# Optimization experiments

Hardware: AMD Instinct MI355X
Metric: run time of the kernel (lower is better)

Reference implementation:

```python
import jax, jax.numpy as jnp
import numpy as np

B, T = 8, 4096
EMBED_DIM = 128
ENGRAM_EMBED_DIM = 64
VOCAB_SIZES = [4096, 4096]
MAX_NGRAM = 3
NUM_HEADS = 2
N_STREAMS = 4
KERNEL = 4
TOTAL_NGRAMS = len(VOCAB_SIZES) * NUM_HEADS          # 4
INPUT_DIM = TOTAL_NGRAMS * ENGRAM_EMBED_DIM          # 256
TOTAL_SLOTS = sum(VOCAB_SIZES) * NUM_HEADS           # 16384


def setup_inputs() -> dict:
    key = jax.random.key(0)
    ks = jax.random.split(key, 10)
    x = jax.random.normal(ks[0], (B, T, N_STREAMS, EMBED_DIM), dtype=jnp.float32)
    input_ids = jax.random.randint(ks[1], (B, T), 0, 50257, dtype=jnp.int32)
    multipliers = jax.random.randint(ks[2], (MAX_NGRAM - 1, NUM_HEADS, MAX_NGRAM), 1, 10000, dtype=jnp.int32)
    embedding = jax.random.normal(ks[3], (TOTAL_SLOTS, ENGRAM_EMBED_DIM), dtype=jnp.float32) * 0.02
    val_W = jax.random.normal(ks[4], (EMBED_DIM, INPUT_DIM), dtype=jnp.float32) * 0.05
    val_b = jnp.zeros((EMBED_DIM,), jnp.float32)
    key_W = jax.random.normal(ks[5], (N_STREAMS, EMBED_DIM, INPUT_DIM), dtype=jnp.float32) * 0.05
    key_b = jnp.zeros((N_STREAMS, EMBED_DIM), jnp.float32)
    normq_w = jnp.ones((N_STREAMS, EMBED_DIM), jnp.float32)
    normk_w = jnp.ones((N_STREAMS, EMBED_DIM), jnp.float32)
    conv_w = jax.random.normal(ks[6], (N_STREAMS * EMBED_DIM, 1, KERNEL), dtype=jnp.float32) * 0.1
    convnorm_w = jnp.ones((N_STREAMS, EMBED_DIM), jnp.float32)
    return {"x": x, "input_ids": input_ids, "multipliers": multipliers,
            "embedding": embedding, "val_W": val_W, "val_b": val_b,
            "key_W": key_W, "key_b": key_b, "normq_w": normq_w,
            "normk_w": normk_w, "conv_w": conv_w, "convnorm_w": convnorm_w}


def rmsnorm(v, w):
    # torch nn.RMSNorm default eps = finfo(dtype).eps
    eps = jnp.finfo(v.dtype).eps
    return v * jax.lax.rsqrt(jnp.mean(v * v, axis=-1, keepdims=True) + eps) * w


def hash_ids_fn(input_ids, multipliers):
    padded = jnp.pad(input_ids, ((0, 0), (MAX_NGRAM - 1, 0)))            # [B, T+2]
    windows = jnp.stack([padded[:, i:i + T] for i in range(MAX_NGRAM)], axis=-1)  # [B,T,3]
    hashes = []
    for n_idx in range(MAX_NGRAM - 1):
        ngram_len = n_idx + 2
        grams = windows[:, :, MAX_NGRAM - ngram_len:]                    # [B,T,L]
        mults = multipliers[n_idx, :, :ngram_len]                        # [H,L]
        mixed = grams[:, :, None, :] * mults[None, None, :, :]           # [B,T,H,L]
        h = mixed[..., 0]
        for k in range(1, ngram_len):
            h = jnp.bitwise_xor(h, mixed[..., k])
        hashes.append(h % VOCAB_SIZES[n_idx])                            # [B,T,H]
    return jnp.concatenate(hashes, axis=2)                               # [B,T,4]


def engram_forward(x, input_ids, multipliers, embedding, val_W, val_b,
                   key_W, key_b, normq_w, normk_w, conv_w, convnorm_w):
    hids = hash_ids_fn(input_ids, multipliers)
    offsets = jnp.cumsum(jnp.array([0] + [v for v in VOCAB_SIZES for _ in range(NUM_HEADS)], jnp.int32))[:-1]
    ids = hids + offsets                                                 # [B,T,4]
    emb = embedding[ids].reshape(B, T, INPUT_DIM)                        # [B,T,256]
    v_base = emb @ val_W.T + val_b                                       # [B,T,128]
    k = rmsnorm(jnp.einsum('bte,gde->btgd', emb, key_W) + key_b, normk_w)  # [B,T,G,D]
    q = rmsnorm(x, normq_w)                                              # [B,T,G,D]
    score = jnp.sum(q * k, axis=-1, keepdims=True) / (EMBED_DIM ** 0.5)
    gates = jax.nn.sigmoid(score)                                        # [B,T,G,1]
    v_gated = v_base[:, :, None, :] * gates                              # [B,T,G,D]
    # ShortConv: per-chunk RMSNorm -> causal depthwise conv -> SiLU
    xn = rmsnorm(v_gated, convnorm_w).reshape(B, T, N_STREAMS * EMBED_DIM)
    x_bct = jnp.transpose(xn, (0, 2, 1))                                 # [B,C,T]
    x_bct = jnp.pad(x_bct, ((0, 0), (0, 0), (KERNEL - 1, 0)))            # causal left pad
    y_bct = jax.lax.conv_general_dilated(
        x_bct, conv_w, window_strides=(1,), padding='VALID',
        dimension_numbers=('NCH', 'OIH', 'NCH'),
        feature_group_count=N_STREAMS * EMBED_DIM)                       # [B,C,T]
    y = jax.nn.silu(y_bct)
    y = jnp.transpose(y, (0, 2, 1)).reshape(B, T, N_STREAMS, EMBED_DIM)
    return v_gated + y


def reference(x, input_ids, multipliers, embedding, val_W, val_b,
              key_W, key_b, normq_w, normk_w, conv_w, convnorm_w):
    return engram_forward(x, input_ids, multipliers, embedding, val_W, val_b,
                          key_W, key_b, normq_w, normk_w, conv_w, convnorm_w)
```

## Files before the change

### kernel.cpp

```cpp
#include <hip/hip_runtime.h>
#include <math.h>

#define EPS 1.1920928955078125e-07f

typedef __attribute__((ext_vector_type(8)))  short short8;
typedef __attribute__((ext_vector_type(4)))  short short4v;
typedef __attribute__((ext_vector_type(16))) float floatx16;

__device__ __forceinline__ float4 ld4(const float* __restrict__ p) { return *(const float4* __restrict__)p; }
__device__ __forceinline__ void   st4(float* __restrict__ p, float4 v) { *(float4* __restrict__)p = v; }

__device__ __forceinline__ unsigned short f2bf(float f) {
    union { float f; unsigned u; } v; v.f = f;
    unsigned r = v.u + 0x7fffu + ((v.u >> 16) & 1u);
    return (unsigned short)(r >> 16);
}

__global__ __launch_bounds__(256) void build_wb(const float* __restrict__ val_W,
                                                const float* __restrict__ key_W,
                                                unsigned short* __restrict__ WbF)
{
    int idx  = blockIdx.x * 256 + threadIdx.x;
    int lane = idx & 63;
    int ks   = (idx >> 6) & 15;
    int nt   = idx >> 10;
    int n = (nt << 5) + (lane & 31);
    int k = (ks << 4) + ((lane >> 5) << 3);
    const float* src = (n < 512) ? key_W + (size_t)n * 256 + k
                                 : val_W + (size_t)(n - 512) * 256 + k;
    float4 v0 = ld4(src), v1 = ld4(src + 4);
    unsigned short o[8] = { f2bf(v0.x), f2bf(v0.y), f2bf(v0.z), f2bf(v0.w),
                            f2bf(v1.x), f2bf(v1.y), f2bf(v1.z), f2bf(v1.w) };
    unsigned short* dst = WbF + (size_t)idx * 8;
    *(short4v*)dst       = *(short4v*)&o[0];
    *(short4v*)(dst + 4) = *(short4v*)&o[4];
}

__global__ __launch_bounds__(256) void engram_gemm(
    const float* __restrict__ x,
    const int*   __restrict__ input_ids,
    const int*   __restrict__ mult,
    const float* __restrict__ embedding,
    const float* __restrict__ val_b,
    const float* __restrict__ key_b,
    const float* __restrict__ normq_w,
    const float* __restrict__ normk_w,
    const unsigned short* __restrict__ WbF,
    float* __restrict__ v_base,
    float* __restrict__ Gbuf,
    float* __restrict__ S2buf)
{
    __shared__ int   sids[64][4];
    __shared__ short AD[64 * 260];

    const int tid  = threadIdx.x;
    const int bid  = blockIdx.x;
    const int c    = bid % 5;
    const int tok0 = (bid / 5) << 6;

    if (tid < 64) {
        int token = tok0 + tid;
        int b = token >> 12, t = token & 4095;
        const int* row = input_ids + (b << 12);
        unsigned g2 = (unsigned)row[t];
        unsigned g1 = (t >= 1) ? (unsigned)row[t - 1] : 0u;
        unsigned g0 = (t >= 2) ? (unsigned)row[t - 2] : 0u;
        sids[tid][0] = (int)(((g1 * (unsigned)mult[0]) ^ (g2 * (unsigned)mult[1])) & 4095u);
        sids[tid][1] = (int)((((g1 * (unsigned)mult[3]) ^ (g2 * (unsigned)mult[4])) & 4095u) + 4096u);
        sids[tid][2] = (int)((((g0 * (unsigned)mult[6]) ^ (g1 * (unsigned)mult[7]) ^ (g2 * (unsigned)mult[8])) & 4095u) + 8192u);
        sids[tid][3] = (int)((((g0 * (unsigned)mult[9]) ^ (g1 * (unsigned)mult[10]) ^ (g2 * (unsigned)mult[11])) & 4095u) + 12288u);
    }
    __syncthreads();

    #pragma unroll
    for (int it = 0; it < 4; ++it) {
        int f = it * 256 + tid;
        int token = f >> 4, seg = f & 15;
        const float* src = embedding + ((size_t)sids[token][seg >> 2] << 6) + ((seg & 3) << 4);
        short* dst = AD + token * 260 + (seg << 4);
        #pragma unroll
        for (int i = 0; i < 4; ++i) {
            float4 v = ld4(src + (i << 2));
            unsigned short o[4] = { f2bf(v.x), f2bf(v.y), f2bf(v.z), f2bf(v.w) };
            *(short4v*)(dst + (i << 2)) = *(short4v*)&o[0];
        }
    }
    __syncthreads();

    const int lane = tid & 63;
    const int wv   = tid >> 6;
    const int half = lane >> 5;
    const int mrow = lane & 31;

    const short* A0 = AD + mrow * 260 + (half << 3);
    const short* A1 = A0 + 32 * 260;
    const float4* Bf = (const float4*)WbF + (size_t)((c * 4 + wv) * 16) * 64 + lane;

    floatx16 acc0, acc1;
    #pragma unroll
    for (int r = 0; r < 16; ++r) { acc0[r] = 0.f; acc1[r] = 0.f; }

    #pragma unroll 4
    for (int ks = 0; ks < 16; ++ks) {
        union { float4 f; short8 s; } ub;
        ub.f = Bf[ks * 64];
        short4v a0l = *(const short4v*)(A0 + (ks << 4));
        short4v a0h = *(const short4v*)(A0 + (ks << 4) + 4);
        short4v a1l = *(const short4v*)(A1 + (ks << 4));
        short4v a1h = *(const short4v*)(A1 + (ks << 4) + 4);
        short8 a0 = { a0l[0], a0l[1], a0l[2], a0l[3], a0h[0], a0h[1], a0h[2], a0h[3] };
        short8 a1 = { a1l[0], a1l[1], a1l[2], a1l[3], a1h[0], a1h[1], a1h[2], a1h[3] };
        acc0 = __builtin_amdgcn_mfma_f32_32x32x16_bf16(a0, ub.s, acc0, 0, 0, 0);
        acc1 = __builtin_amdgcn_mfma_f32_32x32x16_bf16(a1, ub.s, acc1, 0, 0, 0);
    }
    __syncthreads();

    float* D = (float*)AD;
    {
        int colw = (wv << 5) + mrow;
        int rb   = half << 2;
        #pragma unroll
        for (int r = 0; r < 16; ++r) {
            int row = (r & 3) + ((r >> 2) << 3) + rb;
            D[row * 130 + colw]        = acc0[r];
            D[(row + 32) * 130 + colw] = acc1[r];
        }
    }
    __syncthreads();

    const int ty = tid >> 4, tx = tid & 15;
    const int ty4 = ty << 2, tx8 = tx << 3;

    if (c < 4) {
        const int s = c;
        const float* kbp = key_b   + (s << 7) + tx8;
        const float* nqp = normq_w + (s << 7) + tx8;
        const float* nkp = normk_w + (s << 7) + tx8;
        float4 kba = ld4(kbp), kbb = ld4(kbp + 4);
        float4 nqa = ld4(nqp), nqb = ld4(nqp + 4);
        float4 nka = ld4(nkp), nkb = ld4(nkp + 4);
        float kb[8] = {kba.x, kba.y, kba.z, kba.w, kbb.x, kbb.y, kbb.z, kbb.w};
        float nq[8] = {nqa.x, nqa.y, nqa.z, nqa.w, nqb.x, nqb.y, nqb.z, nqb.w};
        float nk[8] = {nka.x, nka.y, nka.z, nka.w, nkb.x, nkb.y, nkb.z, nkb.w};
        #pragma unroll
        for (int j = 0; j < 4; ++j) {
            int t_loc = ty4 + j;
            int token = tok0 + t_loc;
            const float* dp = D + t_loc * 130 + tx8;
            float kr[8]; float ks2 = 0.f;
            #pragma unroll
            for (int m = 0; m < 8; ++m) { kr[m] = dp[m] + kb[m]; ks2 += kr[m] * kr[m]; }
            const float* xp = x + ((((size_t)token << 2) + s) << 7) + tx8;
            float4 xa = ld4(xp), xb = ld4(xp + 4);
            float xv[8] = {xa.x, xa.y, xa.z, xa.w, xb.x, xb.y, xb.z, xb.w};
            float xs2 = 0.f, dt = 0.f;
            #pragma unroll
            for (int m = 0; m < 8; ++m) { xs2 += xv[m] * xv[m]; dt += xv[m] * nq[m] * kr[m] * nk[m]; }
            #pragma unroll
            for (int off = 1; off < 16; off <<= 1) {
                ks2 += __shfl_xor(ks2, off);
                xs2 += __shfl_xor(xs2, off);
                dt  += __shfl_xor(dt,  off);
            }
            float sc = dt * rsqrtf(xs2 * (1.f / 128.f) + EPS)
                          * rsqrtf(ks2 * (1.f / 128.f) + EPS) * 0.08838834764831845f;
            float gate = 1.f / (1.f + expf(-sc));
            if (tx == 0) Gbuf[(token << 2) + s] = gate;
        }
    } else {
        const float* vbp = val_b + tx8;
        float4 vba = ld4(vbp), vbb = ld4(vbp + 4);
        float vb[8] = {vba.x, vba.y, vba.z, vba.w, vbb.x, vbb.y, vbb.z, vbb.w};
        #pragma unroll
        for (int j = 0; j < 4; ++j) {
            int t_loc = ty4 + j;
            int token = tok0 + t_loc;
            const float* dp = D + t_loc * 130 + tx8;
            float v[8]; float s2 = 0.f;
            #pragma unroll
            for (int m = 0; m < 8; ++m) { v[m] = dp[m] + vb[m]; s2 += v[m] * v[m]; }
            #pragma unroll
            for (int off = 1; off < 16; off <<= 1) s2 += __shfl_xor(s2, off);
            float* vp = v_base + ((size_t)token << 7) + tx8;
            st4(vp,     make_float4(v[0], v[1], v[2], v[3]));
            st4(vp + 4, make_float4(v[4], v[5], v[6], v[7]));
            if (tx == 0) S2buf[token] = s2;
        }
    }
}

__global__ __launch_bounds__(256) void engram_out(
    const float* __restrict__ v_base,
    const float* __restrict__ Gbuf,
    const float* __restrict__ S2buf,
    const float* __restrict__ conv_w,
    const float* __restrict__ convnorm_w,
    float* __restrict__ out)
{
    int idx   = blockIdx.x * 256 + threadIdx.x;
    int d4    = idx & 31;
    int token = idx >> 5;
    int t     = token & 4095;

    float vw[4][4];
    float fwin[4][4];
    float gcur[4];
    #pragma unroll
    for (int k = 0; k < 4; ++k) {
        int tt = t + k - 3;
        if (tt >= 0) {
            int tok2 = token + k - 3;
            float4 v = ld4(v_base + ((size_t)tok2 << 7) + (d4 << 2));
            vw[k][0] = v.x; vw[k][1] = v.y; vw[k][2] = v.z; vw[k][3] = v.w;
            float s2n = S2buf[tok2] * (1.f / 128.f);
            #pragma unroll
            for (int s = 0; s < 4; ++s) {
                float g = Gbuf[(tok2 << 2) + s];
                fwin[k][s] = g * rsqrtf(g * g * s2n + EPS);
                if (k == 3) gcur[s] = g;
            }
        } else {
            #pragma unroll
            for (int i = 0; i < 4; ++i) vw[k][i] = 0.f;
            #pragma unroll
            for (int s = 0; s < 4; ++s) fwin[k][s] = 0.f;
        }
    }

    #pragma unroll
    for (int s = 0; s < 4; ++s) {
        float4 cwv = ld4(convnorm_w + (s << 7) + (d4 << 2));
        float cw[4] = {cwv.x, cwv.y, cwv.z, cwv.w};
        float o[4];
        #pragma unroll
        for (int i = 0; i < 4; ++i) {
            const float* wp = conv_w + (size_t)(((s << 7) + (d4 << 2) + i) << 2);
            float4 w = ld4(wp);
            float a = w.x * vw[0][i] * fwin[0][s]
                    + w.y * vw[1][i] * fwin[1][s]
                    + w.z * vw[2][i] * fwin[2][s]
                    + w.w * vw[3][i] * fwin[3][s];
            float y = a * cw[i];
            o[i] = vw[3][i] * gcur[s] + y / (1.f + expf(-y));
        }
        st4(out + ((size_t)((token << 2) + s) << 7) + (d4 << 2),
            make_float4(o[0], o[1], o[2], o[3]));
    }
}

extern "C" void kernel_launch(void* const* d_in, const int* in_sizes, int n_in,
                              void* d_out, int out_size, void* d_ws, size_t ws_size,
                              hipStream_t stream)
{
    const float* x          = (const float*)d_in[0];
    const int*   input_ids  = (const int*)d_in[1];
    const int*   mult       = (const int*)d_in[2];
    const float* embedding  = (const float*)d_in[3];
    const float* val_W      = (const float*)d_in[4];
    const float* val_b      = (const float*)d_in[5];
    const float* key_W      = (const float*)d_in[6];
    const float* key_b      = (const float*)d_in[7];
    const float* normq_w    = (const float*)d_in[8];
    const float* normk_w    = (const float*)d_in[9];
    const float* conv_w     = (const float*)d_in[10];
    const float* convnorm_w = (const float*)d_in[11];
    float* out = (float*)d_out;

    char* ws = (char*)d_ws;
    unsigned short* WbF = (unsigned short*)ws;
    float* v_base = (float*)(ws + 327680);
    float* Gbuf   = (float*)(ws + 327680 + 16777216);
    float* S2buf  = (float*)(ws + 327680 + 16777216 + 524288);

    build_wb<<<80, 256, 0, stream>>>(val_W, key_W, WbF);
    engram_gemm<<<2560, 256, 0, stream>>>(x, input_ids, mult, embedding, val_b, key_b,
                                          normq_w, normk_w, WbF, v_base, Gbuf, S2buf);
    engram_out<<<4096, 256, 0, stream>>>(v_base, Gbuf, S2buf, conv_w, convnorm_w, out);
}
```

Measured before the change: 184.4 us.

## Pre-convert embedding to bf16 and compute all five output tiles per block

Adds a pre-pass that converts the embedding table to bf16 once. Each GEMM block now handles 32 tokens and all five 128-column output chunks (4 key streams plus value), instead of 64 tokens and one chunk. This removes the fivefold redundant gather and bf16 conversion of embedding rows across blocks, at the cost of more accumulator registers, serialized epilogue phases with extra barriers, and an occupancy hint of 4. It also switches expf to the fast __expf.

Result: no change. 185.9 us (+0.8%).

```diff
diff --git a/kernel.cpp b/kernel.cpp
--- a/kernel.cpp
+++ b/kernel.cpp
@@ -36,11 +36,24 @@
     *(short4v*)(dst + 4) = *(short4v*)&o[4];
 }
 
-__global__ __launch_bounds__(256) void engram_gemm(
+__global__ __launch_bounds__(256) void build_ebf(const float* __restrict__ emb,
+                                                 unsigned short* __restrict__ ebf)
+{
+    int idx = blockIdx.x * 256 + threadIdx.x;
+    const float* src = emb + ((size_t)idx << 3);
+    float4 v0 = ld4(src), v1 = ld4(src + 4);
+    unsigned short o[8] = { f2bf(v0.x), f2bf(v0.y), f2bf(v0.z), f2bf(v0.w),
+                            f2bf(v1.x), f2bf(v1.y), f2bf(v1.z), f2bf(v1.w) };
+    unsigned short* dst = ebf + ((size_t)idx << 3);
+    *(short4v*)dst       = *(short4v*)&o[0];
+    *(short4v*)(dst + 4) = *(short4v*)&o[4];
+}
+
+__global__ __launch_bounds__(256, 4) void engram_gemm(
     const float* __restrict__ x,
     const int*   __restrict__ input_ids,
     const int*   __restrict__ mult,
-    const float* __restrict__ embedding,
+    const unsigned short* __restrict__ ebf,
     const float* __restrict__ val_b,
     const float* __restrict__ key_b,
     const float* __restrict__ normq_w,
@@ -50,15 +63,13 @@
     float* __restrict__ Gbuf,
     float* __restrict__ S2buf)
 {
-    __shared__ int   sids[64][4];
-    __shared__ short AD[64 * 260];
+    __shared__ int   sids[32][4];
+    __shared__ short AD[32 * 260];
 
     const int tid  = threadIdx.x;
-    const int bid  = blockIdx.x;
-    const int c    = bid % 5;
-    const int tok0 = (bid / 5) << 6;
-
-    if (tid < 64) {
+    const int tok0 = blockIdx.x << 5;
+
+    if (tid < 32) {
         int token = tok0 + tid;
         int b = token >> 12, t = token & 4095;
         const int* row = input_ids + (b << 12);
@@ -74,16 +85,14 @@
 
     #pragma unroll
     for (int it = 0; it < 4; ++it) {
-        int f = it * 256 + tid;
-        int token = f >> 4, seg = f & 15;
-        const float* src = embedding + ((size_t)sids[token][seg >> 2] << 6) + ((seg & 3) << 4);
-        short* dst = AD + token * 260 + (seg << 4);
-        #pragma unroll
-        for (int i = 0; i < 4; ++i) {
-            float4 v = ld4(src + (i << 2));
-            unsigned short o[4] = { f2bf(v.x), f2bf(v.y), f2bf(v.z), f2bf(v.w) };
-            *(short4v*)(dst + (i << 2)) = *(short4v*)&o[0];
-        }
+        int f = (it << 8) + tid;
+        int token = f >> 5, ch = f & 31;
+        const unsigned short* src = ebf + ((size_t)sids[token][ch >> 3] << 6) + ((ch & 7) << 3);
+        short4v lo = *(const short4v*)src;
+        short4v hi = *(const short4v*)(src + 4);
+        short* dst = AD + token * 260 + (ch << 3);
+        *(short4v*)dst       = lo;
+        *(short4v*)(dst + 4) = hi;
     }
     __syncthreads();
 
@@ -92,99 +101,108 @@
     const int half = lane >> 5;
     const int mrow = lane & 31;
 
-    const short* A0 = AD + mrow * 260 + (half << 3);
-    const short* A1 = A0 + 32 * 260;
-    const float4* Bf = (const float4*)WbF + (size_t)((c * 4 + wv) * 16) * 64 + lane;
-
-    floatx16 acc0, acc1;
-    #pragma unroll
-    for (int r = 0; r < 16; ++r) { acc0[r] = 0.f; acc1[r] = 0.f; }
-
-    #pragma unroll 4
+    const short*  Ap = AD + mrow * 260 + (half << 3);
+    const float4* Bf = (const float4*)WbF + lane;
+
+    floatx16 acc[5];
+    #pragma unroll
+    for (int j = 0; j < 5; ++j)
+        #pragma unroll
+        for (int r = 0; r < 16; ++r) acc[j][r] = 0.f;
+
+    #pragma unroll 2
     for (int ks = 0; ks < 16; ++ks) {
-        union { float4 f; short8 s; } ub;
-        ub.f = Bf[ks * 64];
-        short4v a0l = *(const short4v*)(A0 + (ks << 4));
-        short4v a0h = *(const short4v*)(A0 + (ks << 4) + 4);
-        short4v a1l = *(const short4v*)(A1 + (ks << 4));
-        short4v a1h = *(const short4v*)(A1 + (ks << 4) + 4);
-        short8 a0 = { a0l[0], a0l[1], a0l[2], a0l[3], a0h[0], a0h[1], a0h[2], a0h[3] };
-        short8 a1 = { a1l[0], a1l[1], a1l[2], a1l[3], a1h[0], a1h[1], a1h[2], a1h[3] };
-        acc0 = __builtin_amdgcn_mfma_f32_32x32x16_bf16(a0, ub.s, acc0, 0, 0, 0);
-        acc1 = __builtin_amdgcn_mfma_f32_32x32x16_bf16(a1, ub.s, acc1, 0, 0, 0);
-    }
-    __syncthreads();
-
+        short4v al = *(const short4v*)(Ap + (ks << 4));
+        short4v ah = *(const short4v*)(Ap + (ks << 4) + 4);
+        short8 a = { al[0], al[1], al[2], al[3], ah[0], ah[1], ah[2], ah[3] };
+        #pragma unroll
+        for (int j = 0; j < 5; ++j) {
+            union { float4 f; short8 s; } ub;
+            ub.f = Bf[(size_t)((((wv + (j << 2)) << 4) + ks) << 6)];
+            acc[j] = __builtin_amdgcn_mfma_f32_32x32x16_bf16(a, ub.s, acc[j], 0, 0, 0);
+        }
+    }
+
+    const int ty = tid >> 4, tx = tid & 15;
+    const int tx8 = tx << 3;
     float* D = (float*)AD;
-    {
-        int colw = (wv << 5) + mrow;
-        int rb   = half << 2;
+    const int colw = (wv << 5) + mrow;
+    const int rb   = half << 2;
+
+    #pragma unroll
+    for (int c = 0; c < 5; ++c) {
+        float4 xa0, xb0, xa1, xb1;
+        if (c < 4) {
+            const float* xp0 = x + ((((size_t)(tok0 + (ty << 1))     << 2) + c) << 7) + tx8;
+            const float* xp1 = x + ((((size_t)(tok0 + (ty << 1) + 1) << 2) + c) << 7) + tx8;
+            xa0 = ld4(xp0); xb0 = ld4(xp0 + 4);
+            xa1 = ld4(xp1); xb1 = ld4(xp1 + 4);
+        }
+        __syncthreads();
         #pragma unroll
         for (int r = 0; r < 16; ++r) {
             int row = (r & 3) + ((r >> 2) << 3) + rb;
-            D[row * 130 + colw]        = acc0[r];
-            D[(row + 32) * 130 + colw] = acc1[r];
-        }
-    }
-    __syncthreads();
-
-    const int ty = tid >> 4, tx = tid & 15;
-    const int ty4 = ty << 2, tx8 = tx << 3;
-
-    if (c < 4) {
-        const int s = c;
-        const float* kbp = key_b   + (s << 7) + tx8;
-        const float* nqp = normq_w + (s << 7) + tx8;
-        const float* nkp = normk_w + (s << 7) + tx8;
-        float4 kba = ld4(kbp), kbb = ld4(kbp + 4);
-        float4 nqa = ld4(nqp), nqb = ld4(nqp + 4);
-        float4 nka = ld4(nkp), nkb = ld4(nkp + 4);
-        float kb[8] = {kba.x, kba.y, kba.z, kba.w, kbb.x, kbb.y, kbb.z, kbb.w};
-        float nq[8] = {nqa.x, nqa.y, nqa.z, nqa.w, nqb.x, nqb.y, nqb.z, nqb.w};
-        float nk[8] = {nka.x, nka.y, nka.z, nka.w, nkb.x, nkb.y, nkb.z, nkb.w};
-        #pragma unroll
-        for (int j = 0; j < 4; ++j) {
-            int t_loc = ty4 + j;
-            int token = tok0 + t_loc;
-            const float* dp = D + t_loc * 130 + tx8;
-            float kr[8]; float ks2 = 0.f;
-            #pragma unroll
-            for (int m = 0; m < 8; ++m) { kr[m] = dp[m] + kb[m]; ks2 += kr[m] * kr[m]; }
-            const float* xp = x + ((((size_t)token << 2) + s) << 7) + tx8;
-            float4 xa = ld4(xp), xb = ld4(xp + 4);
-            float xv[8] = {xa.x, xa.y, xa.z, xa.w, xb.x, xb.y, xb.z, xb.w};
-            float xs2 = 0.f, dt = 0.f;
-            #pragma unroll
-            for (int m = 0; m < 8; ++m) { xs2 += xv[m] * xv[m]; dt += xv[m] * nq[m] * kr[m] * nk[m]; }
-            #pragma unroll
-            for (int off = 1; off < 16; off <<= 1) {
-                ks2 += __shfl_xor(ks2, off);
-                xs2 += __shfl_xor(xs2, off);
-                dt  += __shfl_xor(dt,  off);
+            D[row * 130 + colw] = acc[c][r];
+        }
+        __syncthreads();
+
+        if (c < 4) {
+            const int s = c;
+            const float* kbp = key_b   + (s << 7) + tx8;
+            const float* nqp = normq_w + (s << 7) + tx8;
+            const float* nkp = normk_w + (s << 7) + tx8;
+            float4 kba = ld4(kbp), kbb = ld4(kbp + 4);
+            float4 nqa = ld4(nqp), nqb = ld4(nqp + 4);
+            float4 nka = ld4(nkp), nkb = ld4(nkp + 4);
+            float kb[8] = {kba.x, kba.y, kba.z, kba.w, kbb.x, kbb.y, kbb.z, kbb.w};
+            float nq[8] = {nqa.x, nqa.y, nqa.z, nqa.w, nqb.x, nqb.y, nqb.z, nqb.w};
+            float nk[8] = {nka.x, nka.y, nka.z, nka.w, nkb.x, nkb.y, nkb.z, nkb.w};
+            #pragma unroll
+            for (int j = 0; j < 2; ++j) {
+                int t_loc = (ty << 1) + j;
+                int token = tok0 + t_loc;
+                const float* dp = D + t_loc * 130 + tx8;
+                float kr[8]; float ks2 = 0.f;
+                #pragma unroll
+                for (int m = 0; m < 8; ++m) { kr[m] = dp[m] + kb[m]; ks2 += kr[m] * kr[m]; }
+                float xv[8];
+                if (j == 0) { xv[0]=xa0.x; xv[1]=xa0.y; xv[2]=xa0.z; xv[3]=xa0.w;
+                              xv[4]=xb0.x; xv[5]=xb0.y; xv[6]=xb0.z; xv[7]=xb0.w; }
+                else        { xv[0]=xa1.x; xv[1]=xa1.y; xv[2]=xa1.z; xv[3]=xa1.w;
+                              xv[4]=xb1.x; xv[5]=xb1.y; xv[6]=xb1.z; xv[7]=xb1.w; }
+                float xs2 = 0.f, dt = 0.f;
+                #pragma unroll
+                for (int m = 0; m < 8; ++m) { xs2 += xv[m] * xv[m]; dt += xv[m] * nq[m] * kr[m] * nk[m]; }
+                #pragma unroll
+                for (int off = 1; off < 16; off <<= 1) {
+                    ks2 += __shfl_xor(ks2, off);
+                    xs2 += __shfl_xor(xs2, off);
+                    dt  += __shfl_xor(dt,  off);
+                }
+                float sc = dt * rsqrtf(xs2 * (1.f / 128.f) + EPS)
+                              * rsqrtf(ks2 * (1.f / 128.f) + EPS) * 0.08838834764831845f;
+                float gate = 1.f / (1.f + __expf(-sc));
+                if (tx == 0) Gbuf[(token << 2) + s] = gate;
             }
-            float sc = dt * rsqrtf(xs2 * (1.f / 128.f) + EPS)
-                          * rsqrtf(ks2 * (1.f / 128.f) + EPS) * 0.08838834764831845f;
-            float gate = 1.f / (1.f + expf(-sc));
-            if (tx == 0) Gbuf[(token << 2) + s] = gate;
-        }
-    } else {
-        const float* vbp = val_b + tx8;
-        float4 vba = ld4(vbp), vbb = ld4(vbp + 4);
-        float vb[8] = {vba.x, vba.y, vba.z, vba.w, vbb.x, vbb.y, vbb.z, vbb.w};
-        #pragma unroll
-        for (int j = 0; j < 4; ++j) {
-            int t_loc = ty4 + j;
-            int token = tok0 + t_loc;
-            const float* dp = D + t_loc * 130 + tx8;
-            float v[8]; float s2 = 0.f;
-            #pragma unroll
-            for (int m = 0; m < 8; ++m) { v[m] = dp[m] + vb[m]; s2 += v[m] * v[m]; }
-            #pragma unroll
-            for (int off = 1; off < 16; off <<= 1) s2 += __shfl_xor(s2, off);
-            float* vp = v_base + ((size_t)token << 7) + tx8;
-            st4(vp,     make_float4(v[0], v[1], v[2], v[3]));
-            st4(vp + 4, make_float4(v[4], v[5], v[6], v[7]));
-            if (tx == 0) S2buf[token] = s2;
+        } else {
+            const float* vbp = val_b + tx8;
+            float4 vba = ld4(vbp), vbb = ld4(vbp + 4);
+            float vb[8] = {vba.x, vba.y, vba.z, vba.w, vbb.x, vbb.y, vbb.z, vbb.w};
+            #pragma unroll
+            for (int j = 0; j < 2; ++j) {
+                int t_loc = (ty << 1) + j;
+                int token = tok0 + t_loc;
+                const float* dp = D + t_loc * 130 + tx8;
+                float v[8]; float s2 = 0.f;
+                #pragma unroll
+                for (int m = 0; m < 8; ++m) { v[m] = dp[m] + vb[m]; s2 += v[m] * v[m]; }
+                #pragma unroll
+                for (int off = 1; off < 16; off <<= 1) s2 += __shfl_xor(s2, off);
+                float* vp = v_base + ((size_t)token << 7) + tx8;
+                st4(vp,     make_float4(v[0], v[1], v[2], v[3]));
+                st4(vp + 4, make_float4(v[4], v[5], v[6], v[7]));
+                if (tx == 0) S2buf[token] = s2;
+            }
         }
     }
 }
@@ -241,7 +259,7 @@
                     + w.z * vw[2][i] * fwin[2][s]
                     + w.w * vw[3][i] * fwin[3][s];
             float y = a * cw[i];
-            o[i] = vw[3][i] * gcur[s] + y / (1.f + expf(-y));
+            o[i] = vw[3][i] * gcur[s] + y / (1.f + __expf(-y));
         }
         st4(out + ((size_t)((token << 2) + s) << 7) + (d4 << 2),
             make_float4(o[0], o[1], o[2], o[3]));
@@ -268,12 +286,14 @@
 
     char* ws = (char*)d_ws;
     unsigned short* WbF = (unsigned short*)ws;
-    float* v_base = (float*)(ws + 327680);
-    float* Gbuf   = (float*)(ws + 327680 + 16777216);
-    float* S2buf  = (float*)(ws + 327680 + 16777216 + 524288);
+    unsigned short* ebf = (unsigned short*)(ws + 327680);
+    float* v_base = (float*)(ws + 327680 + 2097152);
+    float* Gbuf   = (float*)(ws + 327680 + 2097152 + 16777216);
+    float* S2buf  = (float*)(ws + 327680 + 2097152 + 16777216 + 524288);
 
     build_wb<<<80, 256, 0, stream>>>(val_W, key_W, WbF);
-    engram_gemm<<<2560, 256, 0, stream>>>(x, input_ids, mult, embedding, val_b, key_b,
+    build_ebf<<<512, 256, 0, stream>>>(embedding, ebf);
+    engram_gemm<<<1024, 256, 0, stream>>>(x, input_ids, mult, ebf, val_b, key_b,
                                           normq_w, normk_w, WbF, v_base, Gbuf, S2buf);
     engram_out<<<4096, 256, 0, stream>>>(v_base, Gbuf, S2buf, conv_w, convnorm_w, out);
 }
```
